# Kernel optimization log

Measured on AMD Instinct MI355X. Metric: run time of the kernel, lower is better.

## Reference

```python
import jax, jax.numpy as jnp
import numpy as np

N, D, E, R, K = 8192, 1024, 8, 16, 2  # tokens, d_model, experts, lora rank, top_k


def setup_inputs() -> dict:
    key = jax.random.key(0)
    ks = jax.random.split(key, 6)
    s = 1.0 / np.sqrt(D)
    return {
        "x": jax.random.normal(ks[0], (N, D), jnp.float32),
        "W_gate": jax.random.normal(ks[1], (E, D), jnp.float32) * s,
        "A": jax.random.normal(ks[2], (E, D, R), jnp.float32) * s,
        "B": jax.random.normal(ks[3], (E, R, D), jnp.float32) * (1.0 / np.sqrt(R)),
        "W_base": jax.random.normal(ks[4], (D, D), jnp.float32) * s,
        "b_base": jax.random.normal(ks[5], (D,), jnp.float32) * 0.01,
    }


def reference(x, W_gate, A, B, W_base, b_base):
    # Gating: logits [N, E] -> top-k values/indices, softmax over the k slots
    logits = x @ W_gate.T
    topk_vals, topk_idx = jax.lax.top_k(logits, K)          # [N, K]
    w = jax.nn.softmax(topk_vals.astype(jnp.float32), axis=1).astype(x.dtype)
    # Dense combine weights [N, E]: weight for expert e if selected, else 0
    combine = jnp.sum(jax.nn.one_hot(topk_idx, E, dtype=x.dtype) * w[..., None], axis=1)
    # LoRA experts: expert_e(x) = x @ A_e @ B_e; weighted scatter-add fused via einsum
    h = jnp.einsum('nd,edr->enr', x, A)                     # [E, N, R]
    moe_out = jnp.einsum('enr,erd,ne->nd', h, B, combine)   # [N, D]
    # Base (shared) linear expert, always added when lora_experts=True
    base = x @ W_base.T + b_base
    return moe_out + base
```

## Files before the change

kernel.cpp:

```cpp
#include <hip/hip_runtime.h>
#include <stdint.h>

#define NTOK 8192
#define DM   1024
#define NE   8
#define NR   16
#define KX   1152

typedef short bf16x8 __attribute__((ext_vector_type(8)));
typedef float f32x4  __attribute__((ext_vector_type(4)));

__device__ __forceinline__ unsigned short f2bf(float f) {
    union { float f; unsigned u; } v; v.f = f;
    unsigned r = v.u + 0x7fffu + ((v.u >> 16) & 1u);
    return (unsigned short)(r >> 16);
}

__device__ __forceinline__ void gld16(const void* g, void* l) {
    __builtin_amdgcn_global_load_lds((__attribute__((address_space(1))) void*)g,
                                     (__attribute__((address_space(3))) void*)l,
                                     16, 0, 0);
}

__global__ __launch_bounds__(256) void prep(const float* __restrict__ x,
                                            const float* __restrict__ Wg,
                                            const float* __restrict__ Asrc,
                                            const float* __restrict__ Bsrc,
                                            const float* __restrict__ Wb,
                                            float* __restrict__ combine,
                                            unsigned short* __restrict__ Xext,
                                            unsigned short* __restrict__ WBext,
                                            unsigned short* __restrict__ At) {
    const int b = blockIdx.x;
    const int t = threadIdx.x;

    if (b < 2048) {
        const int lane = t & 63;
        const int w = t >> 6;
        const int n = b * 4 + w;

        const float4* x4 = (const float4*)(x + (size_t)n * DM);
        float4 xv[4];
        #pragma unroll
        for (int i = 0; i < 4; ++i) xv[i] = x4[i * 64 + lane];

        float acc[NE];
        #pragma unroll
        for (int e = 0; e < NE; ++e) {
            const float4* wg4 = (const float4*)(Wg + (size_t)e * DM);
            float s = 0.f;
            #pragma unroll
            for (int i = 0; i < 4; ++i) {
                float4 g = wg4[i * 64 + lane];
                s += xv[i].x * g.x + xv[i].y * g.y + xv[i].z * g.z + xv[i].w * g.w;
            }
            acc[e] = s;
        }
        #pragma unroll
        for (int off = 32; off >= 1; off >>= 1) {
            #pragma unroll
            for (int e = 0; e < NE; ++e) acc[e] += __shfl_xor(acc[e], off, 64);
        }
        float best = acc[0]; int bi = 0;
        #pragma unroll
        for (int e = 1; e < NE; ++e) if (acc[e] > best) { best = acc[e]; bi = e; }
        float sec = -1e30f; int si = 0;
        #pragma unroll
        for (int e = 0; e < NE; ++e) if (e != bi && acc[e] > sec) { sec = acc[e]; si = e; }
        const float ed = __expf(sec - best);
        const float w0 = 1.f / (1.f + ed);
        const float w1 = ed * w0;
        if (lane < NE)
            combine[n * NE + lane] = (lane == bi) ? w0 : ((lane == si) ? w1 : 0.f);

        unsigned short* xrow = Xext + (size_t)n * KX;
        #pragma unroll
        for (int i = 0; i < 4; ++i) {
            ushort4 o;
            o.x = f2bf(xv[i].x); o.y = f2bf(xv[i].y);
            o.z = f2bf(xv[i].z); o.w = f2bf(xv[i].w);
            *(ushort4*)(xrow + (i * 64 + lane) * 4) = o;
        }
    } else if (b < 3072) {
        const int j = b - 2048;
        unsigned short* row = WBext + (size_t)j * KX;
        float4 v = ((const float4*)(Wb + (size_t)j * DM))[t];
        ushort4 o;
        o.x = f2bf(v.x); o.y = f2bf(v.y); o.z = f2bf(v.z); o.w = f2bf(v.w);
        *(ushort4*)(row + t * 4) = o;
        if (t < 128) row[DM + t] = f2bf(Bsrc[(size_t)t * DM + j]);
    } else {
        const int p = b - 3072;
        const int e = p >> 4, r = p & 15;
        for (int d = t; d < DM; d += 256)
            At[(size_t)p * DM + d] = f2bf(Asrc[e * (DM * NR) + d * NR + r]);
    }
}

__global__ __launch_bounds__(256) void hall_kernel(unsigned short* Xext,
                                                   const unsigned short* __restrict__ At,
                                                   const float* __restrict__ combine) {
    __shared__ __align__(16) unsigned short lds[12288];
    const int t = threadIdx.x;
    const int lane = t & 63;
    const int w = t >> 6;
    const int quad = lane >> 4;
    const int l15 = lane & 15;
    const int bid = blockIdx.x;
    const int bm = bid >> 1;
    const int cb = bid & 1;
    const int n0 = bm * 32;
    const int wm = (w & 1) * 16;
    const int wn = (w >> 1) * 32;

    const int srow = t >> 3;
    const int seg  = (t & 7) ^ (srow & 7);

    const unsigned short* gX  = Xext + (size_t)(n0 + srow) * KX + seg * 8;
    const unsigned short* gA0 = At + (size_t)(cb * 64 + srow) * DM + seg * 8;
    const unsigned short* gA1 = At + (size_t)(cb * 64 + 32 + srow) * DM + seg * 8;

    f32x4 acc[2] = {};

    #define HALL_STAGE(k0, s)                                              \
        gld16(gX  + (k0), (char*)lds + (s) * 12288 + w * 1024);            \
        gld16(gA0 + (k0), (char*)lds + (s) * 12288 + 4096 + w * 1024);     \
        gld16(gA1 + (k0), (char*)lds + (s) * 12288 + 8192 + w * 1024);

    #define HALL_COMPUTE(s)                                                        \
        {                                                                          \
            const int xo = (s) * 6144, ao = (s) * 6144 + 2048;                     \
            _Pragma("unroll")                                                      \
            for (int kk = 0; kk < 2; ++kk) {                                       \
                const int gs = kk * 4 + quad;                                      \
                const int sw = (gs ^ (l15 & 7)) * 8;                               \
                bf16x8 a = *(const bf16x8*)&lds[xo + (wm + l15) * 64 + sw];        \
                _Pragma("unroll")                                                  \
                for (int jf = 0; jf < 2; ++jf) {                                   \
                    bf16x8 bb = *(const bf16x8*)&lds[ao + (wn + jf * 16 + l15) * 64 + sw]; \
                    acc[jf] = __builtin_amdgcn_mfma_f32_16x16x32_bf16(a, bb, acc[jf], 0, 0, 0); \
                }                                                                  \
            }                                                                      \
        }

    HALL_STAGE(0, 0);
    for (int k0 = 0; k0 < DM; k0 += 128) {
        __syncthreads();
        HALL_STAGE(k0 + 64, 1);
        HALL_COMPUTE(0);
        __syncthreads();
        if (k0 + 128 < DM) { HALL_STAGE(k0 + 128, 0); }
        HALL_COMPUTE(1);
    }

    #pragma unroll
    for (int jf = 0; jf < 2; ++jf) {
        const int p = cb * 64 + wn + jf * 16 + l15;
        const int e = p >> 4;
        #pragma unroll
        for (int v = 0; v < 4; ++v) {
            const int n = n0 + wm + quad * 4 + v;
            const float val = acc[jf][v] * combine[n * NE + e];
            Xext[(size_t)n * KX + DM + p] = f2bf(val);
        }
    }
    #undef HALL_STAGE
    #undef HALL_COMPUTE
}

__global__ __launch_bounds__(256, 2) void mgemm(const unsigned short* __restrict__ Xext,
                                                const unsigned short* __restrict__ WBext,
                                                const float* __restrict__ bias,
                                                float* __restrict__ out) {
    __shared__ __align__(16) unsigned short lds[32768];
    const int t = threadIdx.x;
    const int lane = t & 63;
    const int w = t >> 6;
    const int quad = lane >> 4;
    const int l15 = lane & 15;

    const int bid = blockIdx.x;
    const int xcd = bid & 7;
    const int loc = bid >> 3;
    const int bm = xcd * 8 + (loc & 7);
    const int bn = loc >> 3;

    const int wm = (w & 1) * 64;
    const int wn = (w >> 1) * 64;

    f32x4 acc[4][4] = {};

    const int srow = t >> 3;
    const int seg  = (t & 7) ^ (srow & 7);
    const unsigned short* gA = Xext  + (size_t)(bm * 128 + srow) * KX + seg * 8;
    const unsigned short* gB = WBext + (size_t)(bn * 128 + srow) * KX + seg * 8;

    #define MG_STAGE(k0, s)                                                          \
        _Pragma("unroll")                                                            \
        for (int c = 0; c < 4; ++c) {                                                \
            gld16(gA + (size_t)c * 32 * KX + (k0), (char*)lds + (s) * 32768 + c * 4096 + w * 1024);        \
            gld16(gB + (size_t)c * 32 * KX + (k0), (char*)lds + (s) * 32768 + 16384 + c * 4096 + w * 1024);\
        }

    #define MG_COMPUTE(s)                                                            \
        {                                                                            \
            const int ao = (s) * 16384, bo = (s) * 16384 + 8192;                     \
            _Pragma("unroll")                                                        \
            for (int kk = 0; kk < 2; ++kk) {                                         \
                const int gs = kk * 4 + quad;                                        \
                const int sw = (gs ^ (l15 & 7)) * 8;                                 \
                bf16x8 a[4], b[4];                                                   \
                _Pragma("unroll")                                                    \
                for (int i = 0; i < 4; ++i)                                          \
                    a[i] = *(const bf16x8*)&lds[ao + (wm + i * 16 + l15) * 64 + sw]; \
                _Pragma("unroll")                                                    \
                for (int j = 0; j < 4; ++j)                                          \
                    b[j] = *(const bf16x8*)&lds[bo + (wn + j * 16 + l15) * 64 + sw]; \
                _Pragma("unroll")                                                    \
                for (int i = 0; i < 4; ++i)                                          \
                    _Pragma("unroll")                                                \
                    for (int j = 0; j < 4; ++j)                                      \
                        acc[i][j] = __builtin_amdgcn_mfma_f32_16x16x32_bf16(a[i], b[j], acc[i][j], 0, 0, 0); \
            }                                                                        \
        }

    MG_STAGE(0, 0);
    for (int k0 = 0; k0 < KX; k0 += 128) {
        __syncthreads();
        MG_STAGE(k0 + 64, 1);
        MG_COMPUTE(0);
        __syncthreads();
        if (k0 + 128 < KX) { MG_STAGE(k0 + 128, 0); }
        MG_COMPUTE(1);
    }
    #undef MG_STAGE
    #undef MG_COMPUTE

    __syncthreads();
    float* lf = (float*)lds + w * 4096;
    #pragma unroll
    for (int j = 0; j < 4; ++j) {
        const float bv = bias[bn * 128 + wn + j * 16 + l15];
        #pragma unroll
        for (int i = 0; i < 4; ++i)
            #pragma unroll
            for (int v = 0; v < 4; ++v) {
                const int row_l = i * 16 + quad * 4 + v;
                const int col_s = (j * 16 + l15) ^ ((row_l & 1) << 4);
                lf[row_l * 64 + col_s] = acc[i][j][v] + bv;
            }
    }
    __builtin_amdgcn_s_waitcnt(0);
    #pragma unroll
    for (int rr = 0; rr < 16; ++rr) {
        const int row_r = rr * 4 + (lane >> 4);
        const int col4  = (lane & 15) * 4;
        const int col4s = col4 ^ ((row_r & 1) << 4);
        float4 vv = *(const float4*)&lf[row_r * 64 + col4s];
        *(float4*)&out[(size_t)(bm * 128 + wm + row_r) * DM + bn * 128 + wn + col4] = vv;
    }
}

extern "C" void kernel_launch(void* const* d_in, const int* in_sizes, int n_in,
                              void* d_out, int out_size, void* d_ws, size_t ws_size,
                              hipStream_t stream) {
    const float* x  = (const float*)d_in[0];
    const float* Wg = (const float*)d_in[1];
    const float* A  = (const float*)d_in[2];
    const float* B  = (const float*)d_in[3];
    const float* Wb = (const float*)d_in[4];
    const float* bb = (const float*)d_in[5];
    float* out = (float*)d_out;

    char* ws = (char*)d_ws;
    float*          combine = (float*)ws;
    unsigned short* Xext    = (unsigned short*)(ws + 262144);
    unsigned short* WBext   = (unsigned short*)(ws + 262144 + 18874368);
    unsigned short* At      = (unsigned short*)(ws + 262144 + 18874368 + 2359296);

    hipLaunchKernelGGL(prep,        dim3(3200), dim3(256), 0, stream,
                       x, Wg, A, B, Wb, combine, Xext, WBext, At);
    hipLaunchKernelGGL(hall_kernel, dim3(512),  dim3(256), 0, stream, Xext, At, combine);
    hipLaunchKernelGGL(mgemm,       dim3(512),  dim3(256), 0, stream, Xext, WBext, bb, out);
}
```

Measured before the change: 129.1 us.

## Fuse gating, x bf16 conversion and LoRA-A projection into one kernel

Gating logits, top-2 softmax, the bf16 conversion of x and the x@A projection now run in a single kernel that streams each fp32 x tile once. Weight preparation moves into its own smaller kernel. This removes the round trip of writing bf16 x and reading it back, and drops the global combine buffer. The cost is that only 256 blocks of 256 threads each cover 32 tokens and all 128 LoRA columns, which may underfill the GPU, and the gate dot products and fp32 loads add per-step latency to the MFMA loop.

```diff
diff --git a/kernel.cpp b/kernel.cpp
--- a/kernel.cpp
+++ b/kernel.cpp
@@ -22,67 +22,15 @@
                                      16, 0, 0);
 }
 
-__global__ __launch_bounds__(256) void prep(const float* __restrict__ x,
-                                            const float* __restrict__ Wg,
-                                            const float* __restrict__ Asrc,
-                                            const float* __restrict__ Bsrc,
-                                            const float* __restrict__ Wb,
-                                            float* __restrict__ combine,
-                                            unsigned short* __restrict__ Xext,
-                                            unsigned short* __restrict__ WBext,
-                                            unsigned short* __restrict__ At) {
+__global__ __launch_bounds__(256) void wprep(const float* __restrict__ Asrc,
+                                             const float* __restrict__ Bsrc,
+                                             const float* __restrict__ Wb,
+                                             unsigned short* __restrict__ WBext,
+                                             unsigned short* __restrict__ At) {
     const int b = blockIdx.x;
     const int t = threadIdx.x;
-
-    if (b < 2048) {
-        const int lane = t & 63;
-        const int w = t >> 6;
-        const int n = b * 4 + w;
-
-        const float4* x4 = (const float4*)(x + (size_t)n * DM);
-        float4 xv[4];
-        #pragma unroll
-        for (int i = 0; i < 4; ++i) xv[i] = x4[i * 64 + lane];
-
-        float acc[NE];
-        #pragma unroll
-        for (int e = 0; e < NE; ++e) {
-            const float4* wg4 = (const float4*)(Wg + (size_t)e * DM);
-            float s = 0.f;
-            #pragma unroll
-            for (int i = 0; i < 4; ++i) {
-                float4 g = wg4[i * 64 + lane];
-                s += xv[i].x * g.x + xv[i].y * g.y + xv[i].z * g.z + xv[i].w * g.w;
-            }
-            acc[e] = s;
-        }
-        #pragma unroll
-        for (int off = 32; off >= 1; off >>= 1) {
-            #pragma unroll
-            for (int e = 0; e < NE; ++e) acc[e] += __shfl_xor(acc[e], off, 64);
-        }
-        float best = acc[0]; int bi = 0;
-        #pragma unroll
-        for (int e = 1; e < NE; ++e) if (acc[e] > best) { best = acc[e]; bi = e; }
-        float sec = -1e30f; int si = 0;
-        #pragma unroll
-        for (int e = 0; e < NE; ++e) if (e != bi && acc[e] > sec) { sec = acc[e]; si = e; }
-        const float ed = __expf(sec - best);
-        const float w0 = 1.f / (1.f + ed);
-        const float w1 = ed * w0;
-        if (lane < NE)
-            combine[n * NE + lane] = (lane == bi) ? w0 : ((lane == si) ? w1 : 0.f);
-
-        unsigned short* xrow = Xext + (size_t)n * KX;
-        #pragma unroll
-        for (int i = 0; i < 4; ++i) {
-            ushort4 o;
-            o.x = f2bf(xv[i].x); o.y = f2bf(xv[i].y);
-            o.z = f2bf(xv[i].z); o.w = f2bf(xv[i].w);
-            *(ushort4*)(xrow + (i * 64 + lane) * 4) = o;
-        }
-    } else if (b < 3072) {
-        const int j = b - 2048;
+    if (b < 1024) {
+        const int j = b;
         unsigned short* row = WBext + (size_t)j * KX;
         float4 v = ((const float4*)(Wb + (size_t)j * DM))[t];
         ushort4 o;
@@ -90,82 +38,145 @@
         *(ushort4*)(row + t * 4) = o;
         if (t < 128) row[DM + t] = f2bf(Bsrc[(size_t)t * DM + j]);
     } else {
-        const int p = b - 3072;
+        const int p = b - 1024;
         const int e = p >> 4, r = p & 15;
         for (int d = t; d < DM; d += 256)
             At[(size_t)p * DM + d] = f2bf(Asrc[e * (DM * NR) + d * NR + r]);
     }
 }
 
-__global__ __launch_bounds__(256) void hall_kernel(unsigned short* Xext,
-                                                   const unsigned short* __restrict__ At,
-                                                   const float* __restrict__ combine) {
-    __shared__ __align__(16) unsigned short lds[12288];
+__global__ __launch_bounds__(256) void gmoe2(const float* __restrict__ x,
+                                             const float* __restrict__ Wg,
+                                             const unsigned short* __restrict__ At,
+                                             unsigned short* __restrict__ Xext) {
+    __shared__ __align__(16) unsigned short lds[20992];
+    float* comb = (float*)(lds + 20480);
+
     const int t = threadIdx.x;
     const int lane = t & 63;
     const int w = t >> 6;
     const int quad = lane >> 4;
     const int l15 = lane & 15;
-    const int bid = blockIdx.x;
-    const int bm = bid >> 1;
-    const int cb = bid & 1;
+    const int bm = blockIdx.x;
     const int n0 = bm * 32;
-    const int wm = (w & 1) * 16;
-    const int wn = (w >> 1) * 32;
-
-    const int srow = t >> 3;
-    const int seg  = (t & 7) ^ (srow & 7);
-
-    const unsigned short* gX  = Xext + (size_t)(n0 + srow) * KX + seg * 8;
-    const unsigned short* gA0 = At + (size_t)(cb * 64 + srow) * DM + seg * 8;
-    const unsigned short* gA1 = At + (size_t)(cb * 64 + 32 + srow) * DM + seg * 8;
-
-    f32x4 acc[2] = {};
-
-    #define HALL_STAGE(k0, s)                                              \
-        gld16(gX  + (k0), (char*)lds + (s) * 12288 + w * 1024);            \
-        gld16(gA0 + (k0), (char*)lds + (s) * 12288 + 4096 + w * 1024);     \
-        gld16(gA1 + (k0), (char*)lds + (s) * 12288 + 8192 + w * 1024);
-
-    #define HALL_COMPUTE(s)                                                        \
+
+    const int r   = t >> 3;
+    const int c8  = t & 7;
+    const int seg = c8 ^ (r & 7);
+
+    const float* gx = x + (size_t)(n0 + r) * DM + seg * 8;
+    unsigned short* xout = Xext + (size_t)(n0 + r) * KX + seg * 8;
+    const unsigned short* gA = At + (size_t)r * DM + seg * 8;
+
+    f32x4 acc[2][2] = {};
+    float gl[NE] = {};
+    float4 u0, u1;
+
+    #define GM_STAGE_AT(k0, s)                                                     \
+        _Pragma("unroll")                                                          \
+        for (int rr = 0; rr < 4; ++rr)                                             \
+            gld16(gA + (size_t)rr * 32 * DM + (k0),                                \
+                  (char*)lds + (s) * 20480 + 4096 + rr * 4096 + w * 1024);
+
+    #define GM_GATE(k0)                                                            \
+        _Pragma("unroll")                                                          \
+        for (int e = 0; e < NE; ++e) {                                             \
+            const float* wp = Wg + (size_t)e * DM + (k0) + seg * 8;                \
+            float4 g0 = *(const float4*)wp;                                        \
+            float4 g1 = *(const float4*)(wp + 4);                                  \
+            gl[e] += u0.x * g0.x + u0.y * g0.y + u0.z * g0.z + u0.w * g0.w         \
+                   + u1.x * g1.x + u1.y * g1.y + u1.z * g1.z + u1.w * g1.w;        \
+        }
+
+    #define GM_XWRITE(k0, s)                                                       \
         {                                                                          \
-            const int xo = (s) * 6144, ao = (s) * 6144 + 2048;                     \
+            bf16x8 xb;                                                             \
+            xb[0] = (short)f2bf(u0.x); xb[1] = (short)f2bf(u0.y);                  \
+            xb[2] = (short)f2bf(u0.z); xb[3] = (short)f2bf(u0.w);                  \
+            xb[4] = (short)f2bf(u1.x); xb[5] = (short)f2bf(u1.y);                  \
+            xb[6] = (short)f2bf(u1.z); xb[7] = (short)f2bf(u1.w);                  \
+            *(bf16x8*)&lds[(s) * 10240 + r * 64 + c8 * 8] = xb;                    \
+            *(bf16x8*)(xout + (k0)) = xb;                                          \
+        }
+
+    #define GM_COMPUTE(s)                                                          \
+        {                                                                          \
+            const int xo = (s) * 10240, ao = (s) * 10240 + 2048;                   \
             _Pragma("unroll")                                                      \
             for (int kk = 0; kk < 2; ++kk) {                                       \
                 const int gs = kk * 4 + quad;                                      \
                 const int sw = (gs ^ (l15 & 7)) * 8;                               \
-                bf16x8 a = *(const bf16x8*)&lds[xo + (wm + l15) * 64 + sw];        \
+                bf16x8 a[2], bb[2];                                                \
+                a[0] = *(const bf16x8*)&lds[xo + l15 * 64 + sw];                   \
+                a[1] = *(const bf16x8*)&lds[xo + (16 + l15) * 64 + sw];            \
+                bb[0] = *(const bf16x8*)&lds[ao + (w * 32 + l15) * 64 + sw];       \
+                bb[1] = *(const bf16x8*)&lds[ao + (w * 32 + 16 + l15) * 64 + sw];  \
                 _Pragma("unroll")                                                  \
-                for (int jf = 0; jf < 2; ++jf) {                                   \
-                    bf16x8 bb = *(const bf16x8*)&lds[ao + (wn + jf * 16 + l15) * 64 + sw]; \
-                    acc[jf] = __builtin_amdgcn_mfma_f32_16x16x32_bf16(a, bb, acc[jf], 0, 0, 0); \
-                }                                                                  \
+                for (int i = 0; i < 2; ++i)                                        \
+                    _Pragma("unroll")                                              \
+                    for (int jf = 0; jf < 2; ++jf)                                 \
+                        acc[i][jf] = __builtin_amdgcn_mfma_f32_16x16x32_bf16(a[i], bb[jf], acc[i][jf], 0, 0, 0); \
             }                                                                      \
         }
 
-    HALL_STAGE(0, 0);
-    for (int k0 = 0; k0 < DM; k0 += 128) {
+    u0 = *(const float4*)gx;
+    u1 = *(const float4*)(gx + 4);
+    GM_GATE(0);
+    GM_XWRITE(0, 0);
+    GM_STAGE_AT(0, 0);
+
+    for (int k = 0; k < 16; ++k) {
+        const int s = k & 1;
         __syncthreads();
-        HALL_STAGE(k0 + 64, 1);
-        HALL_COMPUTE(0);
-        __syncthreads();
-        if (k0 + 128 < DM) { HALL_STAGE(k0 + 128, 0); }
-        HALL_COMPUTE(1);
-    }
-
-    #pragma unroll
-    for (int jf = 0; jf < 2; ++jf) {
-        const int p = cb * 64 + wn + jf * 16 + l15;
-        const int e = p >> 4;
-        #pragma unroll
-        for (int v = 0; v < 4; ++v) {
-            const int n = n0 + wm + quad * 4 + v;
-            const float val = acc[jf][v] * combine[n * NE + e];
-            Xext[(size_t)n * KX + DM + p] = f2bf(val);
-        }
-    }
-    #undef HALL_STAGE
-    #undef HALL_COMPUTE
+        if (k < 15) {
+            const int kn = (k + 1) * 64;
+            GM_STAGE_AT(kn, s ^ 1);
+            u0 = *(const float4*)(gx + kn);
+            u1 = *(const float4*)(gx + kn + 4);
+        }
+        GM_COMPUTE(s);
+        if (k < 15) {
+            const int kn = (k + 1) * 64;
+            GM_GATE(kn);
+            GM_XWRITE(kn, s ^ 1);
+        }
+    }
+    #undef GM_STAGE_AT
+    #undef GM_GATE
+    #undef GM_XWRITE
+    #undef GM_COMPUTE
+
+    #pragma unroll
+    for (int off = 1; off <= 4; off <<= 1)
+        #pragma unroll
+        for (int e = 0; e < NE; ++e) gl[e] += __shfl_xor(gl[e], off, 64);
+    {
+        float best = gl[0]; int bi = 0;
+        #pragma unroll
+        for (int e = 1; e < NE; ++e) if (gl[e] > best) { best = gl[e]; bi = e; }
+        float sec = -1e30f; int si = 0;
+        #pragma unroll
+        for (int e = 0; e < NE; ++e) if (e != bi && gl[e] > sec) { sec = gl[e]; si = e; }
+        const float ed = __expf(sec - best);
+        const float w0 = 1.f / (1.f + ed);
+        const float w1 = ed * w0;
+        comb[r * NE + c8] = (c8 == bi) ? w0 : ((c8 == si) ? w1 : 0.f);
+    }
+    __syncthreads();
+
+    #pragma unroll
+    for (int i = 0; i < 2; ++i)
+        #pragma unroll
+        for (int jf = 0; jf < 2; ++jf) {
+            const int p = w * 32 + jf * 16 + l15;
+            const int e = w * 2 + jf;
+            #pragma unroll
+            for (int v = 0; v < 4; ++v) {
+                const int nl = i * 16 + quad * 4 + v;
+                const float val = acc[i][jf][v] * comb[nl * NE + e];
+                Xext[(size_t)(n0 + nl) * KX + DM + p] = f2bf(val);
+            }
+        }
 }
 
 __global__ __launch_bounds__(256, 2) void mgemm(const unsigned short* __restrict__ Xext,
@@ -273,13 +284,11 @@
     float* out = (float*)d_out;
 
     char* ws = (char*)d_ws;
-    float*          combine = (float*)ws;
-    unsigned short* Xext    = (unsigned short*)(ws + 262144);
-    unsigned short* WBext   = (unsigned short*)(ws + 262144 + 18874368);
-    unsigned short* At      = (unsigned short*)(ws + 262144 + 18874368 + 2359296);
-
-    hipLaunchKernelGGL(prep,        dim3(3200), dim3(256), 0, stream,
-                       x, Wg, A, B, Wb, combine, Xext, WBext, At);
-    hipLaunchKernelGGL(hall_kernel, dim3(512),  dim3(256), 0, stream, Xext, At, combine);
-    hipLaunchKernelGGL(mgemm,       dim3(512),  dim3(256), 0, stream, Xext, WBext, bb, out);
-}
+    unsigned short* Xext  = (unsigned short*)ws;
+    unsigned short* WBext = (unsigned short*)(ws + 18874368);
+    unsigned short* At    = (unsigned short*)(ws + 18874368 + 2359296);
+
+    hipLaunchKernelGGL(wprep, dim3(1152), dim3(256), 0, stream, A, B, Wb, WBext, At);
+    hipLaunchKernelGGL(gmoe2, dim3(256),  dim3(256), 0, stream, x, Wg, At, Xext);
+    hipLaunchKernelGGL(mgemm, dim3(512),  dim3(256), 0, stream, Xext, WBext, bb, out);
+}
```

Result: slower. 139.5 us (+8.0%).
